# Performance work log

Measured on AMD Instinct MI355X. Metric: run time of the kernel, lower is better.

Reference implementation:

```python
import jax, jax.numpy as jnp
import numpy as np

B, IN_DIM, D, P = 256, 1024, 512, 2048


def setup_inputs() -> dict:
    key = jax.random.key(0)
    ks = jax.random.split(key, 7)
    return {
        "x": jax.random.normal(ks[0], (B, IN_DIM), dtype=jnp.float32),
        "y": jax.random.randint(ks[1], (B,), 0, P),
        "Wb": jax.random.normal(ks[2], (D, IN_DIM), dtype=jnp.float32) * 0.02,
        "bb": jax.random.normal(ks[3], (D,), dtype=jnp.float32) * 0.02,
        "Wm": jax.random.normal(ks[4], (P, D), dtype=jnp.float32) * 0.02,
        "bm": jax.random.normal(ks[5], (P,), dtype=jnp.float32) * 0.02,
        "proxies": jax.random.normal(ks[6], (P, D), dtype=jnp.float32),
    }


def reference(x, y, Wb, bb, Wm, bm, proxies):
    # backbone: Linear(in_dim -> D)
    feat = x @ Wb.T + bb                         # [B, D]
    # L2-norm regularizer: mean of per-row L2 norms
    reg_e = jnp.mean(jnp.sqrt(jnp.sum(feat * feat, axis=1)))
    # multi: classification head Linear(D -> P)
    out = feat @ Wm.T + bm                       # [B, P]
    # squared euclidean distance to each proxy (broadcast diff + square + sum)
    den = jnp.sum((feat[:, None, :] - proxies[None, :, :]) ** 2, axis=2)  # [B, P]
    # cross-entropy on negated distances
    logp = jax.nn.log_softmax(-den, axis=1)      # [B, P]
    loss = -jnp.mean(jnp.take_along_axis(logp, y[:, None], axis=1))
    return out, loss, reg_e
```

## Files before the change

### kernel.cpp

```cpp
#include <hip/hip_runtime.h>
#include <hip/hip_bf16.h>
#include <math.h>

#define NB   256
#define KIN  1024
#define ND   512
#define NP   2048
#define NTOT 4096

typedef __bf16 bf16x8 __attribute__((ext_vector_type(8)));
typedef float  f32x4  __attribute__((ext_vector_type(4)));
typedef unsigned short ush8 __attribute__((ext_vector_type(8)));

#define OFF_WPB    0u
#define OFF_FEAT32 4194304u
#define OFF_PN2    4718592u
#define OFF_LOGITS 4726784u
#define OFF_ROWLP  6823936u
#define OFF_ROWNM  6824960u

__device__ __forceinline__ ush8 pack8(float4 f0, float4 f1) {
    union { ush8 v; __hip_bfloat162 h[4]; } o;
    o.h[0] = __float22bfloat162_rn(make_float2(f0.x, f0.y));
    o.h[1] = __float22bfloat162_rn(make_float2(f0.z, f0.w));
    o.h[2] = __float22bfloat162_rn(make_float2(f1.x, f1.y));
    o.h[3] = __float22bfloat162_rn(make_float2(f1.z, f1.w));
    return o.v;
}
__device__ __forceinline__ float4 add4(float4 a, float4 b) {
    return make_float4(a.x + b.x, a.y + b.y, a.z + b.z, a.w + b.w);
}

__global__ __launch_bounds__(256) void k_prep(
    const float* __restrict__ Wm, const float* __restrict__ prox,
    unsigned short* __restrict__ WPb, float* __restrict__ pn2,
    float* __restrict__ feat32)
{
    const int t = threadIdx.x, lane = t & 63, w = t >> 6;
    if (t < 128) feat32[blockIdx.x * 128 + t] = 0.f;
    const int r = blockIdx.x * 4 + w;
    const float* src = (r < NP) ? (Wm + (size_t)r * ND)
                                : (prox + (size_t)(r - NP) * ND);
    float4 v0 = *(const float4*)(src + lane * 8);
    float4 v1 = *(const float4*)(src + lane * 8 + 4);
    *(ush8*)(WPb + (size_t)r * ND + lane * 8) = pack8(v0, v1);
    if (r >= NP) {
        float s = v0.x*v0.x + v0.y*v0.y + v0.z*v0.z + v0.w*v0.w
                + v1.x*v1.x + v1.y*v1.y + v1.z*v1.z + v1.w*v1.w;
#pragma unroll
        for (int off = 32; off; off >>= 1) s += __shfl_down(s, off);
        if (lane == 0) pn2[r - NP] = s;
    }
}

__global__ __launch_bounds__(256) void k_feat(
    const float* __restrict__ x, const float* __restrict__ Wb,
    float* __restrict__ feat32)
{
    __shared__ unsigned short As[2][64 * 32];
    __shared__ unsigned short Bs[2][64 * 32];
    const int t = threadIdx.x, lane = t & 63, w = t >> 6;
    const int n0 = blockIdx.x * 64, m0 = blockIdx.y * 64, k0 = blockIdx.z * 128;
    const int srow = t >> 2, sc = (t & 3) * 8;
    const float* gA = x  + (size_t)(m0 + srow) * KIN + k0 + sc;
    const float* gB = Wb + (size_t)(n0 + srow) * KIN + k0 + sc;
    float4 a0 = *(const float4*)gA, a1 = *(const float4*)(gA + 4);
    float4 b0 = *(const float4*)gB, b1 = *(const float4*)(gB + 4);
    f32x4 acc[2][2] = {};
    const int wm = (w >> 1) * 32, wn = (w & 1) * 32;
    const int arow = wm + (lane & 15), brow = wn + (lane & 15);
    const int fcol = (lane >> 4) * 8;
#pragma unroll
    for (int ks = 0; ks < 4; ++ks) {
        *(ush8*)&As[ks & 1][srow * 32 + sc] = pack8(a0, a1);
        *(ush8*)&Bs[ks & 1][srow * 32 + sc] = pack8(b0, b1);
        __syncthreads();
        if (ks + 1 < 4) {
            a0 = *(const float4*)(gA + (ks + 1) * 32);
            a1 = *(const float4*)(gA + (ks + 1) * 32 + 4);
            b0 = *(const float4*)(gB + (ks + 1) * 32);
            b1 = *(const float4*)(gB + (ks + 1) * 32 + 4);
        }
        const unsigned short* as = &As[ks & 1][0];
        const unsigned short* bs = &Bs[ks & 1][0];
        bf16x8 af0 = *(const bf16x8*)&as[(arow     ) * 32 + fcol];
        bf16x8 af1 = *(const bf16x8*)&as[(arow + 16) * 32 + fcol];
        bf16x8 bf0 = *(const bf16x8*)&bs[(brow     ) * 32 + fcol];
        bf16x8 bf1 = *(const bf16x8*)&bs[(brow + 16) * 32 + fcol];
        acc[0][0] = __builtin_amdgcn_mfma_f32_16x16x32_bf16(af0, bf0, acc[0][0], 0, 0, 0);
        acc[0][1] = __builtin_amdgcn_mfma_f32_16x16x32_bf16(af0, bf1, acc[0][1], 0, 0, 0);
        acc[1][0] = __builtin_amdgcn_mfma_f32_16x16x32_bf16(af1, bf0, acc[1][0], 0, 0, 0);
        acc[1][1] = __builtin_amdgcn_mfma_f32_16x16x32_bf16(af1, bf1, acc[1][1], 0, 0, 0);
    }
    const int q = lane >> 4, cn = lane & 15;
#pragma unroll
    for (int i = 0; i < 2; ++i)
#pragma unroll
        for (int j = 0; j < 2; ++j) {
            const int n = n0 + wn + 16 * j + cn;
#pragma unroll
            for (int r = 0; r < 4; ++r) {
                const int m = m0 + wm + 16 * i + q * 4 + r;
                atomicAdd(&feat32[m * ND + n], acc[i][j][r]);
            }
        }
}

__global__ __launch_bounds__(256) void k_head(
    const float* __restrict__ feat32, const float* __restrict__ bb,
    const unsigned short* __restrict__ WPb,
    const float* __restrict__ bm, const float* __restrict__ pn2,
    float* __restrict__ out, float* __restrict__ logits)
{
    __shared__ unsigned short As[2][64 * 32];
    __shared__ unsigned short Bs[2][64 * 32];
    const int t = threadIdx.x, lane = t & 63, w = t >> 6;
    const int n0 = blockIdx.x * 64;
    const int m0 = blockIdx.y * 64;
    const int srow = t >> 2, sc = (t & 3) * 8;
    const float*          gA = feat32 + (size_t)(m0 + srow) * ND + sc;
    const unsigned short* gB = WPb    + (size_t)(n0 + srow) * ND + sc;
    float4 a0 = *(const float4*)gA, a1 = *(const float4*)(gA + 4);
    float4 u0 = *(const float4*)(bb + sc), u1 = *(const float4*)(bb + sc + 4);
    ush8 vb = *(const ush8*)gB;
    f32x4 acc[2][2] = {};
    const int wm = (w >> 1) * 32, wn = (w & 1) * 32;
    const int fr = lane & 15, fcol = (lane >> 4) * 8;
    for (int ks = 0; ks < ND / 32; ++ks) {
        *(ush8*)&As[ks & 1][srow * 32 + sc] = pack8(add4(a0, u0), add4(a1, u1));
        *(ush8*)&Bs[ks & 1][srow * 32 + sc] = vb;
        __syncthreads();
        if (ks + 1 < ND / 32) {
            a0 = *(const float4*)(gA + (ks + 1) * 32);
            a1 = *(const float4*)(gA + (ks + 1) * 32 + 4);
            u0 = *(const float4*)(bb + (ks + 1) * 32 + sc);
            u1 = *(const float4*)(bb + (ks + 1) * 32 + sc + 4);
            vb = *(const ush8*)(gB + (ks + 1) * 32);
        }
        const unsigned short* as = &As[ks & 1][0];
        const unsigned short* bs = &Bs[ks & 1][0];
        bf16x8 af0 = *(const bf16x8*)&as[(wm      + fr) * 32 + fcol];
        bf16x8 af1 = *(const bf16x8*)&as[(wm + 16 + fr) * 32 + fcol];
        bf16x8 bf0 = *(const bf16x8*)&bs[(wn      + fr) * 32 + fcol];
        bf16x8 bf1 = *(const bf16x8*)&bs[(wn + 16 + fr) * 32 + fcol];
        acc[0][0] = __builtin_amdgcn_mfma_f32_16x16x32_bf16(af0, bf0, acc[0][0], 0, 0, 0);
        acc[0][1] = __builtin_amdgcn_mfma_f32_16x16x32_bf16(af0, bf1, acc[0][1], 0, 0, 0);
        acc[1][0] = __builtin_amdgcn_mfma_f32_16x16x32_bf16(af1, bf0, acc[1][0], 0, 0, 0);
        acc[1][1] = __builtin_amdgcn_mfma_f32_16x16x32_bf16(af1, bf1, acc[1][1], 0, 0, 0);
    }
    const bool isProxy = (n0 >= NP);
    const int q = lane >> 4;
#pragma unroll
    for (int i = 0; i < 2; ++i)
#pragma unroll
        for (int j = 0; j < 2; ++j) {
            const int n = n0 + wn + 16 * j + fr;
            const float cadd = isProxy ? pn2[n - NP] : bm[n];
#pragma unroll
            for (int r = 0; r < 4; ++r) {
                const int m = m0 + wm + 16 * i + q * 4 + r;
                const float v = acc[i][j][r];
                if (isProxy) logits[m * NP + (n - NP)] = 2.0f * v - cadd;
                else         out[m * NP + n] = v + cadd;
            }
        }
}

__device__ __forceinline__ float block_reduce(float v, float* sred, int op)
{
    const int lane = threadIdx.x & 63, wave = threadIdx.x >> 6;
#pragma unroll
    for (int off = 32; off; off >>= 1) {
        float o = __shfl_down(v, off);
        v = op ? fmaxf(v, o) : (v + o);
    }
    if (lane == 0) sred[wave] = v;
    __syncthreads();
    if (threadIdx.x == 0) {
        float r = sred[0];
#pragma unroll
        for (int wv = 1; wv < 4; ++wv) r = op ? fmaxf(r, sred[wv]) : (r + sred[wv]);
        sred[0] = r;
    }
    __syncthreads();
    float r = sred[0];
    __syncthreads();
    return r;
}

__global__ __launch_bounds__(256) void k_loss(
    const float* __restrict__ feat32, const float* __restrict__ bb,
    const float* __restrict__ logits, const int* __restrict__ y,
    float* __restrict__ rowlp, float* __restrict__ rownm)
{
    __shared__ float sred[4];
    const int b = blockIdx.x, t = threadIdx.x;

    float v0 = feat32[b * ND + t] + bb[t];
    float v1 = feat32[b * ND + t + 256] + bb[t + 256];
    float fn2 = block_reduce(v0 * v0 + v1 * v1, sred, 0);

    const float* lr = logits + (size_t)b * NP;
    float lv[8], mx = -INFINITY;
#pragma unroll
    for (int j = 0; j < 8; ++j) { lv[j] = lr[t + 256 * j]; mx = fmaxf(mx, lv[j]); }
    float MX = block_reduce(mx, sred, 1);
    float es = 0.f;
#pragma unroll
    for (int j = 0; j < 8; ++j) es += __expf(lv[j] - MX);
    float SUM = block_reduce(es, sred, 0);

    if (t == 0) {
        float ly = lr[y[b]];
        rowlp[b] = ly - MX - __logf(SUM);
        rownm[b] = sqrtf(fn2);
    }
}

__global__ __launch_bounds__(256) void k_final(
    const float* __restrict__ rowlp, const float* __restrict__ rownm,
    float* __restrict__ tail)
{
    __shared__ float sred[4];
    const int t = threadIdx.x;
    float s1 = block_reduce(rowlp[t], sred, 0);
    float s2 = block_reduce(rownm[t], sred, 0);
    if (t == 0) {
        tail[0] = -s1 / (float)NB;
        tail[1] =  s2 / (float)NB;
    }
}

extern "C" void kernel_launch(void* const* d_in, const int* in_sizes, int n_in,
                              void* d_out, int out_size, void* d_ws, size_t ws_size,
                              hipStream_t stream)
{
    const float* x       = (const float*)d_in[0];
    const int*   y       = (const int*)  d_in[1];
    const float* Wb      = (const float*)d_in[2];
    const float* bb      = (const float*)d_in[3];
    const float* Wm      = (const float*)d_in[4];
    const float* bm      = (const float*)d_in[5];
    const float* proxies = (const float*)d_in[6];

    char* ws = (char*)d_ws;
    unsigned short* WPb    = (unsigned short*)(ws + OFF_WPB);
    float*          feat32 = (float*)(ws + OFF_FEAT32);
    float*          pn2    = (float*)(ws + OFF_PN2);
    float*          logits = (float*)(ws + OFF_LOGITS);
    float*          rowlp  = (float*)(ws + OFF_ROWLP);
    float*          rownm  = (float*)(ws + OFF_ROWNM);

    float* out  = (float*)d_out;
    float* tail = out + (size_t)NB * NP;

    k_prep <<<dim3(NTOT / 4), dim3(256), 0, stream>>>(Wm, proxies, WPb, pn2, feat32);
    k_feat <<<dim3(ND / 64, NB / 64, 8), dim3(256), 0, stream>>>(x, Wb, feat32);
    k_head <<<dim3(NTOT / 64, NB / 64), dim3(256), 0, stream>>>(
        feat32, bb, WPb, bm, pn2, out, logits);
    k_loss <<<dim3(NB), dim3(256), 0, stream>>>(feat32, bb, logits, y, rowlp, rownm);
    k_final<<<dim3(1), dim3(256), 0, stream>>>(rowlp, rownm, tail);
}
```

Baseline: 97.60 us.

## Fuse weight prep with feature GEMM and fold final reduction into loss kernel

Merges the weight/proxy bf16 conversion into the feature GEMM launch as extra blocks, replaces the split-K atomic feature GEMM with a full-K tile that writes bias-added fp32 and bf16 features directly, and pre-scales proxies by two so the head epilogue drops a multiply. The final reduction kernel is removed by atomically accumulating loss and norm means into the output tail, cutting five launches to three. Tradeoffs are only 32 GEMM blocks each running a 32-step K loop, which lowers parallelism for the feature GEMM, and atomic float accumulation, which makes the summation order nondeterministic.

```diff
diff --git a/kernel.cpp b/kernel.cpp
--- a/kernel.cpp
+++ b/kernel.cpp
@@ -14,10 +14,9 @@
 
 #define OFF_WPB    0u
 #define OFF_FEAT32 4194304u
-#define OFF_PN2    4718592u
-#define OFF_LOGITS 4726784u
-#define OFF_ROWLP  6823936u
-#define OFF_ROWNM  6824960u
+#define OFF_FEATB  4718592u
+#define OFF_PN2    4980736u
+#define OFF_LOGITS 4988928u
 
 __device__ __forceinline__ ush8 pack8(float4 f0, float4 f1) {
     union { ush8 v; __hip_bfloat162 h[4]; } o;
@@ -27,115 +26,71 @@
     o.h[3] = __float22bfloat162_rn(make_float2(f1.z, f1.w));
     return o.v;
 }
-__device__ __forceinline__ float4 add4(float4 a, float4 b) {
-    return make_float4(a.x + b.x, a.y + b.y, a.z + b.z, a.w + b.w);
-}
-
-__global__ __launch_bounds__(256) void k_prep(
+__device__ __forceinline__ unsigned short f2bf(float v) {
+    union { __hip_bfloat16 h; unsigned short u; } c;
+    c.h = __float2bfloat16(v);
+    return c.u;
+}
+
+__global__ __launch_bounds__(256) void k_fa(
+    const float* __restrict__ x, const float* __restrict__ Wb,
+    const float* __restrict__ bb,
     const float* __restrict__ Wm, const float* __restrict__ prox,
     unsigned short* __restrict__ WPb, float* __restrict__ pn2,
-    float* __restrict__ feat32)
-{
-    const int t = threadIdx.x, lane = t & 63, w = t >> 6;
-    if (t < 128) feat32[blockIdx.x * 128 + t] = 0.f;
-    const int r = blockIdx.x * 4 + w;
-    const float* src = (r < NP) ? (Wm + (size_t)r * ND)
-                                : (prox + (size_t)(r - NP) * ND);
-    float4 v0 = *(const float4*)(src + lane * 8);
-    float4 v1 = *(const float4*)(src + lane * 8 + 4);
-    *(ush8*)(WPb + (size_t)r * ND + lane * 8) = pack8(v0, v1);
-    if (r >= NP) {
-        float s = v0.x*v0.x + v0.y*v0.y + v0.z*v0.z + v0.w*v0.w
-                + v1.x*v1.x + v1.y*v1.y + v1.z*v1.z + v1.w*v1.w;
-#pragma unroll
-        for (int off = 32; off; off >>= 1) s += __shfl_down(s, off);
-        if (lane == 0) pn2[r - NP] = s;
-    }
-}
-
-__global__ __launch_bounds__(256) void k_feat(
-    const float* __restrict__ x, const float* __restrict__ Wb,
-    float* __restrict__ feat32)
+    float* __restrict__ feat32, unsigned short* __restrict__ featb,
+    float* __restrict__ tail)
 {
     __shared__ unsigned short As[2][64 * 32];
     __shared__ unsigned short Bs[2][64 * 32];
     const int t = threadIdx.x, lane = t & 63, w = t >> 6;
-    const int n0 = blockIdx.x * 64, m0 = blockIdx.y * 64, k0 = blockIdx.z * 128;
+
+    if (blockIdx.x >= 32) {
+        const int pb = blockIdx.x - 32;
+        if (pb == 0 && t < 2) tail[t] = 0.f;
+#pragma unroll
+        for (int i = 0; i < 4; ++i) {
+            const int r = pb * 16 + w * 4 + i;
+            const float* src = (r < NP) ? (Wm + (size_t)r * ND)
+                                        : (prox + (size_t)(r - NP) * ND);
+            float4 v0 = *(const float4*)(src + lane * 8);
+            float4 v1 = *(const float4*)(src + lane * 8 + 4);
+            if (r < NP) {
+                *(ush8*)(WPb + (size_t)r * ND + lane * 8) = pack8(v0, v1);
+            } else {
+                float s = v0.x*v0.x + v0.y*v0.y + v0.z*v0.z + v0.w*v0.w
+                        + v1.x*v1.x + v1.y*v1.y + v1.z*v1.z + v1.w*v1.w;
+#pragma unroll
+                for (int off = 32; off; off >>= 1) s += __shfl_down(s, off);
+                if (lane == 0) pn2[r - NP] = s;
+                float4 d0 = make_float4(v0.x + v0.x, v0.y + v0.y,
+                                        v0.z + v0.z, v0.w + v0.w);
+                float4 d1 = make_float4(v1.x + v1.x, v1.y + v1.y,
+                                        v1.z + v1.z, v1.w + v1.w);
+                *(ush8*)(WPb + (size_t)r * ND + lane * 8) = pack8(d0, d1);
+            }
+        }
+        return;
+    }
+
+    const int m0 = (blockIdx.x >> 3) * 64, n0 = (blockIdx.x & 7) * 64;
     const int srow = t >> 2, sc = (t & 3) * 8;
-    const float* gA = x  + (size_t)(m0 + srow) * KIN + k0 + sc;
-    const float* gB = Wb + (size_t)(n0 + srow) * KIN + k0 + sc;
+    const float* gA = x  + (size_t)(m0 + srow) * KIN + sc;
+    const float* gB = Wb + (size_t)(n0 + srow) * KIN + sc;
     float4 a0 = *(const float4*)gA, a1 = *(const float4*)(gA + 4);
     float4 b0 = *(const float4*)gB, b1 = *(const float4*)(gB + 4);
     f32x4 acc[2][2] = {};
     const int wm = (w >> 1) * 32, wn = (w & 1) * 32;
-    const int arow = wm + (lane & 15), brow = wn + (lane & 15);
-    const int fcol = (lane >> 4) * 8;
-#pragma unroll
-    for (int ks = 0; ks < 4; ++ks) {
+    const int fr = lane & 15, fcol = (lane >> 4) * 8;
+
+    for (int ks = 0; ks < KIN / 32; ++ks) {
         *(ush8*)&As[ks & 1][srow * 32 + sc] = pack8(a0, a1);
         *(ush8*)&Bs[ks & 1][srow * 32 + sc] = pack8(b0, b1);
         __syncthreads();
-        if (ks + 1 < 4) {
+        if (ks + 1 < KIN / 32) {
             a0 = *(const float4*)(gA + (ks + 1) * 32);
             a1 = *(const float4*)(gA + (ks + 1) * 32 + 4);
             b0 = *(const float4*)(gB + (ks + 1) * 32);
             b1 = *(const float4*)(gB + (ks + 1) * 32 + 4);
-        }
-        const unsigned short* as = &As[ks & 1][0];
-        const unsigned short* bs = &Bs[ks & 1][0];
-        bf16x8 af0 = *(const bf16x8*)&as[(arow     ) * 32 + fcol];
-        bf16x8 af1 = *(const bf16x8*)&as[(arow + 16) * 32 + fcol];
-        bf16x8 bf0 = *(const bf16x8*)&bs[(brow     ) * 32 + fcol];
-        bf16x8 bf1 = *(const bf16x8*)&bs[(brow + 16) * 32 + fcol];
-        acc[0][0] = __builtin_amdgcn_mfma_f32_16x16x32_bf16(af0, bf0, acc[0][0], 0, 0, 0);
-        acc[0][1] = __builtin_amdgcn_mfma_f32_16x16x32_bf16(af0, bf1, acc[0][1], 0, 0, 0);
-        acc[1][0] = __builtin_amdgcn_mfma_f32_16x16x32_bf16(af1, bf0, acc[1][0], 0, 0, 0);
-        acc[1][1] = __builtin_amdgcn_mfma_f32_16x16x32_bf16(af1, bf1, acc[1][1], 0, 0, 0);
-    }
-    const int q = lane >> 4, cn = lane & 15;
-#pragma unroll
-    for (int i = 0; i < 2; ++i)
-#pragma unroll
-        for (int j = 0; j < 2; ++j) {
-            const int n = n0 + wn + 16 * j + cn;
-#pragma unroll
-            for (int r = 0; r < 4; ++r) {
-                const int m = m0 + wm + 16 * i + q * 4 + r;
-                atomicAdd(&feat32[m * ND + n], acc[i][j][r]);
-            }
-        }
-}
-
-__global__ __launch_bounds__(256) void k_head(
-    const float* __restrict__ feat32, const float* __restrict__ bb,
-    const unsigned short* __restrict__ WPb,
-    const float* __restrict__ bm, const float* __restrict__ pn2,
-    float* __restrict__ out, float* __restrict__ logits)
-{
-    __shared__ unsigned short As[2][64 * 32];
-    __shared__ unsigned short Bs[2][64 * 32];
-    const int t = threadIdx.x, lane = t & 63, w = t >> 6;
-    const int n0 = blockIdx.x * 64;
-    const int m0 = blockIdx.y * 64;
-    const int srow = t >> 2, sc = (t & 3) * 8;
-    const float*          gA = feat32 + (size_t)(m0 + srow) * ND + sc;
-    const unsigned short* gB = WPb    + (size_t)(n0 + srow) * ND + sc;
-    float4 a0 = *(const float4*)gA, a1 = *(const float4*)(gA + 4);
-    float4 u0 = *(const float4*)(bb + sc), u1 = *(const float4*)(bb + sc + 4);
-    ush8 vb = *(const ush8*)gB;
-    f32x4 acc[2][2] = {};
-    const int wm = (w >> 1) * 32, wn = (w & 1) * 32;
-    const int fr = lane & 15, fcol = (lane >> 4) * 8;
-    for (int ks = 0; ks < ND / 32; ++ks) {
-        *(ush8*)&As[ks & 1][srow * 32 + sc] = pack8(add4(a0, u0), add4(a1, u1));
-        *(ush8*)&Bs[ks & 1][srow * 32 + sc] = vb;
-        __syncthreads();
-        if (ks + 1 < ND / 32) {
-            a0 = *(const float4*)(gA + (ks + 1) * 32);
-            a1 = *(const float4*)(gA + (ks + 1) * 32 + 4);
-            u0 = *(const float4*)(bb + (ks + 1) * 32 + sc);
-            u1 = *(const float4*)(bb + (ks + 1) * 32 + sc + 4);
-            vb = *(const ush8*)(gB + (ks + 1) * 32);
         }
         const unsigned short* as = &As[ks & 1][0];
         const unsigned short* bs = &Bs[ks & 1][0];
@@ -148,6 +103,64 @@
         acc[1][0] = __builtin_amdgcn_mfma_f32_16x16x32_bf16(af1, bf0, acc[1][0], 0, 0, 0);
         acc[1][1] = __builtin_amdgcn_mfma_f32_16x16x32_bf16(af1, bf1, acc[1][1], 0, 0, 0);
     }
+
+    const int q = lane >> 4;
+#pragma unroll
+    for (int i = 0; i < 2; ++i)
+#pragma unroll
+        for (int j = 0; j < 2; ++j) {
+            const int n = n0 + wn + 16 * j + fr;
+            const float bbn = bb[n];
+#pragma unroll
+            for (int r = 0; r < 4; ++r) {
+                const int m = m0 + wm + 16 * i + q * 4 + r;
+                const float v = acc[i][j][r] + bbn;
+                feat32[m * ND + n] = v;
+                featb [m * ND + n] = f2bf(v);
+            }
+        }
+}
+
+__global__ __launch_bounds__(256) void k_fb(
+    const unsigned short* __restrict__ featb,
+    const unsigned short* __restrict__ WPb,
+    const float* __restrict__ bm, const float* __restrict__ pn2,
+    float* __restrict__ out, float* __restrict__ logits)
+{
+    __shared__ unsigned short As[2][64 * 32];
+    __shared__ unsigned short Bs[2][64 * 32];
+    const int t = threadIdx.x, lane = t & 63, w = t >> 6;
+    const int n0 = blockIdx.x * 64;
+    const int m0 = blockIdx.y * 64;
+    const int srow = t >> 2, sc = (t & 3) * 8;
+    const unsigned short* gA = featb + (size_t)(m0 + srow) * ND + sc;
+    const unsigned short* gB = WPb   + (size_t)(n0 + srow) * ND + sc;
+    ush8 va = *(const ush8*)gA;
+    ush8 vb = *(const ush8*)gB;
+    f32x4 acc[2][2] = {};
+    const int wm = (w >> 1) * 32, wn = (w & 1) * 32;
+    const int fr = lane & 15, fcol = (lane >> 4) * 8;
+
+    for (int ks = 0; ks < ND / 32; ++ks) {
+        *(ush8*)&As[ks & 1][srow * 32 + sc] = va;
+        *(ush8*)&Bs[ks & 1][srow * 32 + sc] = vb;
+        __syncthreads();
+        if (ks + 1 < ND / 32) {
+            va = *(const ush8*)(gA + (ks + 1) * 32);
+            vb = *(const ush8*)(gB + (ks + 1) * 32);
+        }
+        const unsigned short* as = &As[ks & 1][0];
+        const unsigned short* bs = &Bs[ks & 1][0];
+        bf16x8 af0 = *(const bf16x8*)&as[(wm      + fr) * 32 + fcol];
+        bf16x8 af1 = *(const bf16x8*)&as[(wm + 16 + fr) * 32 + fcol];
+        bf16x8 bf0 = *(const bf16x8*)&bs[(wn      + fr) * 32 + fcol];
+        bf16x8 bf1 = *(const bf16x8*)&bs[(wn + 16 + fr) * 32 + fcol];
+        acc[0][0] = __builtin_amdgcn_mfma_f32_16x16x32_bf16(af0, bf0, acc[0][0], 0, 0, 0);
+        acc[0][1] = __builtin_amdgcn_mfma_f32_16x16x32_bf16(af0, bf1, acc[0][1], 0, 0, 0);
+        acc[1][0] = __builtin_amdgcn_mfma_f32_16x16x32_bf16(af1, bf0, acc[1][0], 0, 0, 0);
+        acc[1][1] = __builtin_amdgcn_mfma_f32_16x16x32_bf16(af1, bf1, acc[1][1], 0, 0, 0);
+    }
+
     const bool isProxy = (n0 >= NP);
     const int q = lane >> 4;
 #pragma unroll
@@ -160,7 +173,7 @@
             for (int r = 0; r < 4; ++r) {
                 const int m = m0 + wm + 16 * i + q * 4 + r;
                 const float v = acc[i][j][r];
-                if (isProxy) logits[m * NP + (n - NP)] = 2.0f * v - cadd;
+                if (isProxy) logits[m * NP + (n - NP)] = v - cadd;
                 else         out[m * NP + n] = v + cadd;
             }
         }
@@ -188,16 +201,15 @@
     return r;
 }
 
-__global__ __launch_bounds__(256) void k_loss(
-    const float* __restrict__ feat32, const float* __restrict__ bb,
-    const float* __restrict__ logits, const int* __restrict__ y,
-    float* __restrict__ rowlp, float* __restrict__ rownm)
+__global__ __launch_bounds__(256) void k_fc(
+    const float* __restrict__ feat32, const float* __restrict__ logits,
+    const int* __restrict__ y, float* __restrict__ tail)
 {
     __shared__ float sred[4];
     const int b = blockIdx.x, t = threadIdx.x;
 
-    float v0 = feat32[b * ND + t] + bb[t];
-    float v1 = feat32[b * ND + t + 256] + bb[t + 256];
+    float v0 = feat32[b * ND + t];
+    float v1 = feat32[b * ND + t + 256];
     float fn2 = block_reduce(v0 * v0 + v1 * v1, sred, 0);
 
     const float* lr = logits + (size_t)b * NP;
@@ -212,22 +224,9 @@
 
     if (t == 0) {
         float ly = lr[y[b]];
-        rowlp[b] = ly - MX - __logf(SUM);
-        rownm[b] = sqrtf(fn2);
-    }
-}
-
-__global__ __launch_bounds__(256) void k_final(
-    const float* __restrict__ rowlp, const float* __restrict__ rownm,
-    float* __restrict__ tail)
-{
-    __shared__ float sred[4];
-    const int t = threadIdx.x;
-    float s1 = block_reduce(rowlp[t], sred, 0);
-    float s2 = block_reduce(rownm[t], sred, 0);
-    if (t == 0) {
-        tail[0] = -s1 / (float)NB;
-        tail[1] =  s2 / (float)NB;
+        float lp = ly - MX - __logf(SUM);
+        atomicAdd(&tail[0], -lp * (1.0f / (float)NB));
+        atomicAdd(&tail[1], sqrtf(fn2) * (1.0f / (float)NB));
     }
 }
 
@@ -246,18 +245,16 @@
     char* ws = (char*)d_ws;
     unsigned short* WPb    = (unsigned short*)(ws + OFF_WPB);
     float*          feat32 = (float*)(ws + OFF_FEAT32);
+    unsigned short* featb  = (unsigned short*)(ws + OFF_FEATB);
     float*          pn2    = (float*)(ws + OFF_PN2);
     float*          logits = (float*)(ws + OFF_LOGITS);
-    float*          rowlp  = (float*)(ws + OFF_ROWLP);
-    float*          rownm  = (float*)(ws + OFF_ROWNM);
 
     float* out  = (float*)d_out;
     float* tail = out + (size_t)NB * NP;
 
-    k_prep <<<dim3(NTOT / 4), dim3(256), 0, stream>>>(Wm, proxies, WPb, pn2, feat32);
-    k_feat <<<dim3(ND / 64, NB / 64, 8), dim3(256), 0, stream>>>(x, Wb, feat32);
-    k_head <<<dim3(NTOT / 64, NB / 64), dim3(256), 0, stream>>>(
-        feat32, bb, WPb, bm, pn2, out, logits);
-    k_loss <<<dim3(NB), dim3(256), 0, stream>>>(feat32, bb, logits, y, rowlp, rownm);
-    k_final<<<dim3(1), dim3(256), 0, stream>>>(rowlp, rownm, tail);
-}
+    k_fa<<<dim3(288), dim3(256), 0, stream>>>(
+        x, Wb, bb, Wm, proxies, WPb, pn2, feat32, featb, tail);
+    k_fb<<<dim3(NTOT / 64, NB / 64), dim3(256), 0, stream>>>(
+        featb, WPb, bm, pn2, out, logits);
+    k_fc<<<dim3(NB), dim3(256), 0, stream>>>(feat32, logits, y, tail);
+}
```

Result: slower. 108.7 us (+11.3%).
